# Performance work log

Hardware: AMD Instinct MI355X
Metric: run time of the kernel (lower is better)

The kernel has to match this reference:

```python
import jax, jax.numpy as jnp
import numpy as np

KS = 3        # kernel_size
STRIDE = 1    # patch_stride
RATE = 2      # compression_rate
SCALE = 10.0  # softmax_scale
FUSE_K = 3    # fuse_kernel
EPS = 1e-9
RAW_K = 2 * RATE


def _pad_same(x, k, stride, dilation):
    # TF-style SAME zero padding, matching the torch module's same_pad.
    H, W = x.shape[-2], x.shape[-1]
    oh, ow = -(-H // stride), -(-W // stride)
    eff = (k - 1) * dilation + 1
    ph = max(0, (oh - 1) * stride + eff - H)
    pw = max(0, (ow - 1) * stride + eff - W)
    pads = [(0, 0)] * (x.ndim - 2) + [(ph // 2, ph - ph // 2), (pw // 2, pw - pw // 2)]
    return jnp.pad(x, pads), oh, ow


def extract_patches(x, k, stride, dilation):
    # x: [B,C,H,W] -> [B, L, C, k, k]; L row-major over output grid (== torch Unfold + view/permute)
    xp, oh, ow = _pad_same(x, k, stride, dilation)
    B, C = x.shape[0], x.shape[1]
    cols = [xp[:, :,
               i * dilation: i * dilation + (oh - 1) * stride + 1: stride,
               j * dilation: j * dilation + (ow - 1) * stride + 1: stride]
            for i in range(k) for j in range(k)]
    p = jnp.stack(cols, axis=2).reshape(B, C, k, k, oh * ow)
    return p.transpose(0, 4, 1, 2, 3), oh, ow


def _diag_fuse(x):
    # SAME conv of a 2D map with an eye(FUSE_K) kernel == sum of FUSE_K diagonal shifts.
    pad = FUSE_K - 1
    t = pad // 2
    xp = jnp.pad(x, ((t, pad - t), (t, pad - t)))
    return sum(xp[d:d + x.shape[0], d:d + x.shape[1]] for d in range(FUSE_K))


def _forward(fg, bg, mask):
    B, C, H, W = fg.shape
    # raw (full-res) background patches -> transpose-conv reconstruction weights  [B,L,C,4,4]
    wr, _, _ = extract_patches(bg, RAW_K, RATE * STRIDE, RATE)
    # nearest downsample by RATE (torch F.interpolate nearest, scale 1/RATE)
    fgd = fg[:, :, ::RATE, ::RATE]
    bgd = bg[:, :, ::RATE, ::RATE]
    hd, wd = fgd.shape[2], fgd.shape[3]
    # matching weights from downsampled background  [B,L,C,3,3]
    w, _, _ = extract_patches(bgd, KS, STRIDE, 1)
    # mask resized (nearest) to downsampled grid, patch means  [B,L]
    md = mask[:, :, ::H // hd, ::W // wd]
    mp, _, _ = extract_patches(md, KS, STRIDE, 1)
    m = jnp.mean(mp, axis=(2, 3, 4))
    # foreground patches (SAME, stride 1) for the dynamic-weight conv  [B,Lf,C,3,3]
    fp, _, _ = extract_patches(fgd, KS, 1, 1)

    def per_sample(fp_i, w_i, wr_i, m_i):
        # L2-normalize each background patch (eps added per element, as in torch code)
        norm = jnp.sqrt(jnp.sum(w_i ** 2 + EPS, axis=(1, 2, 3), keepdims=True))
        wn = w_i / norm
        # conv2d(fg, weight) == patch-matching GEMM: sim[l, q] over fg positions q
        sim = jnp.einsum('qcij,lcij->lq', fp_i, wn)  # [L, Lf]
        # fuse: diagonal smoothing along both (bg-patch, fg-pixel) axis pairings
        s = _diag_fuse(sim)
        s = s.reshape(hd, wd, hd, wd).transpose(1, 0, 3, 2).reshape(wd * hd, wd * hd)
        s = _diag_fuse(s)
        sim = s.reshape(wd, hd, wd, hd).transpose(1, 0, 3, 2).reshape(hd * wd, hd, wd)
        mi = m_i[:, None, None]
        sim = jax.nn.softmax(sim * mi * SCALE, axis=0) * mi  # softmax over L
        # conv_transpose2d(sim, wr, stride=RATE) via lhs-dilated conv with flipped kernel
        wk = jnp.flip(wr_i, axis=(2, 3)).transpose(1, 0, 2, 3)  # [C, L, 4, 4]
        y = jax.lax.conv_general_dilated(
            sim[None], wk, window_strides=(1, 1),
            padding=[(RAW_K - 1, RAW_K - 1)] * 2,
            lhs_dilation=(RATE, RATE),
            dimension_numbers=('NCHW', 'OIHW', 'NCHW'))
        return y[0, :, :H, :W] / float(RAW_K ** 2)

    return jax.vmap(per_sample)(fp, w, wr, m)  # [B, C, H, W]


def setup_inputs() -> dict:
    key = jax.random.key(0)
    k1, k2, k3 = jax.random.split(key, 3)
    B, C, H, W = 4, 96, 96, 96
    fg = jax.random.normal(k1, (B, C, H, W), dtype=jnp.float32)
    bg = jax.random.normal(k2, (B, C, H, W), dtype=jnp.float32)
    mask = jnp.round(jax.random.uniform(k3, (B, 1, H, W), dtype=jnp.float32))
    return {"fg": fg, "bg": bg, "mask": mask}


def reference(fg, bg, mask):
    return _forward(fg, bg, mask)
```

## Files before the change

kernel.cpp:

```cpp
#include <hip/hip_runtime.h>
#include <hip/hip_bf16.h>
#include <cstdint>
#include <cstring>

#define ND 48
#define LQ 2304
#define CCH 96
#define HWD 96
#define CHW (CCH*HWD*HWD)
#define HW2 (HWD*HWD)
#define K2P 2560
#define NJ2 384
#define KSP 384

typedef __attribute__((ext_vector_type(8))) short bf16x8;
typedef __attribute__((ext_vector_type(4))) float f32x4;

__device__ __forceinline__ float4 ld4u(const float* p) {
  float4 v; __builtin_memcpy(&v, p, 16); return v;
}

__global__ void k_down(const float* __restrict__ fg, const float* __restrict__ bg,
                       float* __restrict__ fgdT, float* __restrict__ bgdT,
                       float* __restrict__ n2, size_t sd, size_t sp) {
  int b = blockIdx.z;
  const float* fgb = fg + (size_t)b * CHW;
  const float* bgb = bg + (size_t)b * CHW;
  float* fT = fgdT + (size_t)b * sd;
  float* bT = bgdT + (size_t)b * sd;
  float* n2b = n2 + (size_t)b * sp;
  int p = blockIdx.x * 256 + threadIdx.x;
  if (p >= LQ) return;
  int py = p / ND, px = p % ND;
  const float* fsrc = fgb + (2 * py) * HWD + 2 * px;
  const float* gsrc = bgb + (2 * py) * HWD + 2 * px;
  float s = 0.f;
  for (int c = 0; c < CCH; ++c) {
    float f = fsrc[c * HW2];
    float g = gsrc[c * HW2];
    fT[c * LQ + p] = f;
    bT[c * LQ + p] = g;
    s += g * g;
  }
  n2b[p] = s;
}

__global__ void k_aux(const float* __restrict__ n2, const float* __restrict__ mask,
                      float* __restrict__ rnorm, float* __restrict__ mval, size_t sp) {
  int b = blockIdx.z;
  const float* n2b = n2 + (size_t)b * sp;
  const float* mb = mask + (size_t)b * HW2;
  float* rn = rnorm + (size_t)b * sp;
  float* mv = mval + (size_t)b * sp;
  int p = blockIdx.x * 256 + threadIdx.x;
  if (p >= LQ) return;
  int py = p / ND, px = p % ND;
  float ssq = 0.f, ms = 0.f;
  for (int dy = -1; dy <= 1; ++dy)
    for (int dx = -1; dx <= 1; ++dx) {
      int yy = py + dy, xx = px + dx;
      if (yy >= 0 && yy < ND && xx >= 0 && xx < ND) {
        ssq += n2b[yy * ND + xx];
        ms  += mb[(2 * yy) * HWD + 2 * xx];
      }
    }
  rn[p] = 1.0f / sqrtf(ssq + 864.0f * 1e-9f);
  mv[p] = ms * (1.0f / 9.0f);
}

__global__ __launch_bounds__(256) void k_split(const float* __restrict__ fgdT,
                                               const float* __restrict__ bgdT,
                                               __hip_bfloat16* __restrict__ AB,
                                               size_t sd, size_t sAB) {
  int b = blockIdx.z;
  const float* fT = fgdT + (size_t)b * sd;
  const float* gT = bgdT + (size_t)b * sd;
  __hip_bfloat16* Ao = AB + (size_t)b * sAB;
  __hip_bfloat16* Bo = Ao + (size_t)LQ * KSP;
  __shared__ float fs[96 * 65], gs[96 * 65];
  int q0 = blockIdx.x * 64;
  int tid = threadIdx.x;
#pragma unroll
  for (int i = 0; i < 24; ++i) {
    int e = i * 256 + tid;
    int c = e >> 6, qq = e & 63;
    fs[c * 65 + qq] = fT[c * LQ + q0 + qq];
    gs[c * 65 + qq] = gT[c * LQ + q0 + qq];
  }
  __syncthreads();
  for (int i = 0; i < 24; ++i) {
    int e = i * 256 + tid;
    int qq = e / 96, k4 = (e % 96) * 4;
    unsigned short a4[4], b4[4];
    if (k4 < 288) {
      int part = k4 / 96, c = k4 % 96;
#pragma unroll
      for (int j = 0; j < 4; ++j) {
        float f = fs[(c + j) * 65 + qq];
        float g = gs[(c + j) * 65 + qq];
        __hip_bfloat16 fh = __float2bfloat16(f);
        __hip_bfloat16 gh = __float2bfloat16(g);
        __hip_bfloat16 fl = __float2bfloat16(f - __bfloat162float(fh));
        __hip_bfloat16 gl = __float2bfloat16(g - __bfloat162float(gh));
        __hip_bfloat16 av = (part == 2) ? fl : fh;
        __hip_bfloat16 bv = (part == 1) ? gl : gh;
        a4[j] = *(unsigned short*)&av;
        b4[j] = *(unsigned short*)&bv;
      }
    } else {
      a4[0] = a4[1] = a4[2] = a4[3] = 0;
      b4[0] = b4[1] = b4[2] = b4[3] = 0;
    }
    __builtin_memcpy(&Ao[(size_t)(q0 + qq) * KSP + k4], a4, 8);
    __builtin_memcpy(&Bo[(size_t)(q0 + qq) * KSP + k4], b4, 8);
  }
}

__device__ __forceinline__ void gload16(const void* g, void* l) {
  __builtin_amdgcn_global_load_lds((const __attribute__((address_space(1))) void*)g,
                                   (__attribute__((address_space(3))) void*)l, 16, 0, 0);
}

__global__ __launch_bounds__(256) void k_rgemm_mfma(const __hip_bfloat16* __restrict__ AB,
                                                    float* __restrict__ R,
                                                    size_t sAB, size_t sR) {
  int bz = blockIdx.z;
  const __hip_bfloat16* Aq = AB + (size_t)bz * sAB;
  const __hip_bfloat16* Bq = Aq + (size_t)LQ * KSP;
  float* Rb = R + (size_t)bz * sR;
  __shared__ __align__(16) __hip_bfloat16 As[2][64 * 128];
  __shared__ __align__(16) __hip_bfloat16 Bs[2][64 * 128];
  int m0 = blockIdx.y * 64, n0 = blockIdx.x * 64;
  int tid = threadIdx.x;
  int w = tid >> 6, lane = tid & 63;
  int wm = w >> 1, wn = w & 1;
  f32x4 acc[2][2] = {};

  auto STAGE = [&](int buf, int k0) {
#pragma unroll
    for (int i = 0; i < 4; ++i) {
      int g = i * 256 + tid;
      int row = g >> 4, slot = g & 15;
      int ks = 8 * (slot ^ (row & 7));
      gload16(Aq + (size_t)(m0 + row) * KSP + k0 + ks, &As[buf][g * 8]);
      gload16(Bq + (size_t)(n0 + row) * KSP + k0 + ks, &Bs[buf][g * 8]);
    }
  };

  STAGE(0, 0);
  __syncthreads();
  int cur = 0;
  for (int t = 0; t < 3; ++t) {
    if (t + 1 < 3) STAGE(cur ^ 1, (t + 1) * 128);
#pragma unroll
    for (int kk = 0; kk < 128; kk += 32) {
      bf16x8 af[2], bfr[2];
#pragma unroll
      for (int mi = 0; mi < 2; ++mi) {
        int row = wm * 32 + mi * 16 + (lane & 15);
        int e = (kk + (lane >> 4) * 8) ^ ((row & 7) * 8);
        af[mi] = *(const bf16x8*)(&As[cur][row * 128 + e]);
      }
#pragma unroll
      for (int ni = 0; ni < 2; ++ni) {
        int row = wn * 32 + ni * 16 + (lane & 15);
        int e = (kk + (lane >> 4) * 8) ^ ((row & 7) * 8);
        bfr[ni] = *(const bf16x8*)(&Bs[cur][row * 128 + e]);
      }
#pragma unroll
      for (int mi = 0; mi < 2; ++mi)
#pragma unroll
        for (int ni = 0; ni < 2; ++ni)
          acc[mi][ni] = __builtin_amdgcn_mfma_f32_16x16x32_bf16(af[mi], bfr[ni], acc[mi][ni], 0, 0, 0);
    }
    __syncthreads();
    cur ^= 1;
  }

#pragma unroll
  for (int mi = 0; mi < 2; ++mi)
#pragma unroll
    for (int ni = 0; ni < 2; ++ni)
#pragma unroll
      for (int rr = 0; rr < 4; ++rr) {
        int row = m0 + wm * 32 + mi * 16 + (lane >> 4) * 4 + rr;
        int col = n0 + wn * 32 + ni * 16 + (lane & 15);
        Rb[(size_t)row * LQ + col] = acc[mi][ni][rr];
      }
}

__global__ void k_t9v(const float* __restrict__ R, const float* __restrict__ rnorm,
                      float* __restrict__ A2, size_t sR, size_t sp) {
  int b = blockIdx.z;
  const float* S = R + (size_t)b * sR;
  const float* rn = rnorm + (size_t)b * sp;
  float* O = A2 + (size_t)b * sR;
  int bid = blockIdx.x;
  int wg = (bid & 7) * 648 + (bid >> 3);
  int t = wg * 256 + threadIdx.x;
  int id = t * 4;
  int q = id / LQ, l = id % LQ;
  int qy = q / ND, qx = q % ND;
  int ly = l / ND, lx0 = l % ND;
  float4 acc = make_float4(0.f, 0.f, 0.f, 0.f);
#pragma unroll
  for (int dy = -1; dy <= 1; ++dy) {
    if (qy + dy < 0 || qy + dy >= ND || ly + dy < 0 || ly + dy >= ND) continue;
#pragma unroll
    for (int dx = -1; dx <= 1; ++dx) {
      if (qx + dx < 0 || qx + dx >= ND) continue;
      int off = (dy * ND + dx) * (LQ + 1);
      float4 m = ld4u(S + id + off);
      if (dx == -1 && lx0 == 0) m.x = 0.f;
      if (dx == 1 && lx0 == ND - 4) m.w = 0.f;
      acc.x += m.x; acc.y += m.y; acc.z += m.z; acc.w += m.w;
    }
  }
  float4 r4 = *(const float4*)(rn + l);
  acc.x *= r4.x; acc.y *= r4.y; acc.z *= r4.z; acc.w *= r4.w;
  *(float4*)(O + id) = acc;
}

__global__ void k_fusev(const float* __restrict__ A2, float* __restrict__ F, size_t sR) {
  int b = blockIdx.z;
  const float* S = A2 + (size_t)b * sR;
  float* Fo = F + (size_t)b * sR;
  int bid = blockIdx.x;
  int wg = (bid & 7) * 648 + (bid >> 3);
  int t = wg * 256 + threadIdx.x;
  int id = t * 4;
  int a = id / LQ, bc0 = id % LQ;
  float4 c = *(const float4*)(S + id);
  if (a > 0) {
    float4 m = ld4u(S + id - LQ - 1);
    if (bc0 == 0) m.x = 0.f;
    c.x += m.x; c.y += m.y; c.z += m.z; c.w += m.w;
  }
  if (a < LQ - 1) {
    float4 p = ld4u(S + id + LQ + 1);
    if (bc0 == LQ - 4) p.w = 0.f;
    c.x += p.x; c.y += p.y; c.z += p.z; c.w += p.w;
  }
  *(float4*)(Fo + id) = c;
}

__global__ __launch_bounds__(256) void k_softmax(const float* __restrict__ F,
                                                 const float* __restrict__ mval,
                                                 __hip_bfloat16* __restrict__ P50s,
                                                 size_t sR, size_t sp, size_t sP) {
  int b = blockIdx.z;
  const float* Fb = F + (size_t)b * sR;
  const float* mv = mval + (size_t)b * sp;
  __hip_bfloat16* Pb = P50s + (size_t)b * sP + K2P;
  int bid = blockIdx.x;
  int q = (bid & 7) * 288 + (bid >> 3);
  int qy = q / ND, qx = q % ND;
  int tid = threadIdx.x;
  __shared__ float wred[8];
  int fq0 = qx * ND + qy - 1, fq2 = qx * ND + qy + 1;
  bool qok0 = (fq0 >= 0), qok2 = (fq2 < LQ);
  const float* pm = Fb + (size_t)(qok0 ? (fq0 % ND) * ND + fq0 / ND : 0) * LQ;
  const float* pc = Fb + (size_t)q * LQ;
  const float* pp = Fb + (size_t)(qok2 ? (fq2 % ND) * ND + fq2 / ND : 0) * LQ;

  float lg[3][4], mq[3][4];
  float vmax = -1e30f;
#pragma unroll
  for (int s = 0; s < 3; ++s) {
    int Qi = s * 256 + tid;
    bool act = (Qi < 576);
    if (act) {
      int l = Qi * 4;
      int ly = l / ND, lx0 = l % ND;
      float4 acc = *(const float4*)(pc + l);
      if (qok0) {
        float4 t0 = (ly > 0) ? ld4u(pm + l - ND) : ld4u(pm + 2255 + lx0);
        if (ly == 0 && lx0 == 0) t0.x = 0.f;
        acc.x += t0.x; acc.y += t0.y; acc.z += t0.z; acc.w += t0.w;
      }
      if (qok2) {
        float4 t2 = (ly < ND - 1) ? ld4u(pp + l + ND) : ld4u(pp + lx0 + 1);
        if (ly == ND - 1 && lx0 == ND - 4) t2.w = 0.f;
        acc.x += t2.x; acc.y += t2.y; acc.z += t2.z; acc.w += t2.w;
      }
      float4 m4 = *(const float4*)(mv + l);
      mq[s][0] = m4.x; mq[s][1] = m4.y; mq[s][2] = m4.z; mq[s][3] = m4.w;
      lg[s][0] = acc.x * 10.0f * m4.x;
      lg[s][1] = acc.y * 10.0f * m4.y;
      lg[s][2] = acc.z * 10.0f * m4.z;
      lg[s][3] = acc.w * 10.0f * m4.w;
#pragma unroll
      for (int j = 0; j < 4; ++j) vmax = fmaxf(vmax, lg[s][j]);
    } else {
#pragma unroll
      for (int j = 0; j < 4; ++j) { lg[s][j] = -1e30f; mq[s][j] = 0.f; }
    }
  }
#pragma unroll
  for (int d = 32; d; d >>= 1) vmax = fmaxf(vmax, __shfl_xor(vmax, d));
  int wv = tid >> 6, lane = tid & 63;
  if (lane == 0) wred[wv] = vmax;
  __syncthreads();
  vmax = fmaxf(fmaxf(wred[0], wred[1]), fmaxf(wred[2], wred[3]));
  float ssum = 0.f;
#pragma unroll
  for (int s = 0; s < 3; ++s)
#pragma unroll
    for (int j = 0; j < 4; ++j) { lg[s][j] = __expf(lg[s][j] - vmax); ssum += lg[s][j]; }
#pragma unroll
  for (int d = 32; d; d >>= 1) ssum += __shfl_xor(ssum, d);
  if (lane == 0) wred[4 + wv] = ssum;
  __syncthreads();
  float inv = 1.0f / (wred[4] + wred[5] + wred[6] + wred[7]);
#pragma unroll
  for (int s = 0; s < 3; ++s) {
    int Qi = s * 256 + tid;
    if (Qi >= 576) continue;
    int l = Qi * 4;
    int ly = l / ND;
    size_t base = (size_t)q * K2P + l + 2 * ly;
    unsigned int u01, u23;
    {
      __hip_bfloat16 h0 = __float2bfloat16(lg[s][0] * inv * mq[s][0]);
      __hip_bfloat16 h1 = __float2bfloat16(lg[s][1] * inv * mq[s][1]);
      unsigned short s0, s1;
      __builtin_memcpy(&s0, &h0, 2); __builtin_memcpy(&s1, &h1, 2);
      u01 = (unsigned int)s0 | ((unsigned int)s1 << 16);
      __hip_bfloat16 h2 = __float2bfloat16(lg[s][2] * inv * mq[s][2]);
      __hip_bfloat16 h3 = __float2bfloat16(lg[s][3] * inv * mq[s][3]);
      unsigned short s2, s3;
      __builtin_memcpy(&s2, &h2, 2); __builtin_memcpy(&s3, &h3, 2);
      u23 = (unsigned int)s2 | ((unsigned int)s3 << 16);
    }
    *(unsigned int*)((unsigned short*)Pb + base) = u01;
    *(unsigned int*)((unsigned short*)Pb + base + 2) = u23;
  }
  __hip_bfloat16 z = __float2bfloat16(0.f);
  int pc2;
  if (tid < 96)        pc2 = (tid >> 1) * 50 + ND + (tid & 1);
  else if (tid < 196)  pc2 = 2400 + (tid - 96);
  else                 pc2 = 2500 + (tid - 196);
  Pb[(size_t)q * K2P + pc2] = z;
  if (q == 0)
    for (int i = tid; i < K2P; i += 256) (Pb - K2P)[i] = z;
}

__global__ void k_q2v(const __hip_bfloat16* __restrict__ P50s,
                      __hip_bfloat16* __restrict__ Q2, size_t sP, size_t sQ) {
  int bz = blockIdx.z;
  const __hip_bfloat16* P = P50s + (size_t)bz * sP + K2P;
  __hip_bfloat16* Q = Q2 + (size_t)bz * sQ;
  int bid = blockIdx.x;
  int wg = (bid & 7) * 360 + (bid >> 3);
  int id = wg * 256 + threadIdx.x;
  int r = id / 320, c8 = (id % 320) * 8;
  int a = r / ND, b = r % ND;
  const __hip_bfloat16* base = P + (size_t)r * K2P + c8;
  float acc[8];
  {
    unsigned short s[8]; __builtin_memcpy(s, base, 16);
#pragma unroll
    for (int i = 0; i < 8; ++i) {
      unsigned int u = ((unsigned int)s[i]) << 16;
      acc[i] = __builtin_bit_cast(float, u);
    }
  }
  if (b >= 1) {
    unsigned short s[8]; __builtin_memcpy(s, base - (K2P + 2), 16);
#pragma unroll
    for (int i = 0; i < 8; ++i) {
      unsigned int u = ((unsigned int)s[i]) << 16;
      acc[i] += __builtin_bit_cast(float, u);
    }
  }
  if (a >= 1) {
    unsigned short s[8]; __builtin_memcpy(s, base - (ND * K2P + 100), 16);
#pragma unroll
    for (int i = 0; i < 8; ++i) {
      unsigned int u = ((unsigned int)s[i]) << 16;
      acc[i] += __builtin_bit_cast(float, u);
    }
  }
  if (a >= 1 && b >= 1) {
    unsigned short s[8]; __builtin_memcpy(s, base - ((ND + 1) * K2P + 102), 16);
#pragma unroll
    for (int i = 0; i < 8; ++i) {
      unsigned int u = ((unsigned int)s[i]) << 16;
      acc[i] += __builtin_bit_cast(float, u);
    }
  }
  __hip_bfloat16 o[8];
#pragma unroll
  for (int i = 0; i < 8; ++i) o[i] = __float2bfloat16(acc[i]);
  *(bf16x8*)(Q + (size_t)r * K2P + c8) = *(bf16x8*)o;
}

__global__ void k_b2(const float* __restrict__ bgdT, __hip_bfloat16* __restrict__ B2,
                     size_t sd, size_t sB) {
  int b = blockIdx.z;
  const float* gT = bgdT + (size_t)b * sd;
  __hip_bfloat16* Bb = B2 + (size_t)b * sB;
  int id = blockIdx.x * 256 + threadIdx.x;
  if (id >= NJ2 * K2P) return;
  int j = id / K2P, col = id % K2P;
  int c = j >> 2, s = (j >> 1) & 1, t = j & 1;
  float v = 0.f;
  if (col < 2500) {
    int m = col / 50, n = col % 50;
    int ry = m + s - 1, rx = n + t - 1;
    if (ry >= 0 && ry < ND && rx >= 0 && rx < ND)
      v = gT[c * LQ + ry * ND + rx];
  }
  Bb[id] = __float2bfloat16(v);
}

__global__ __launch_bounds__(256) void k_gemm3(const __hip_bfloat16* __restrict__ A,
                                               const __hip_bfloat16* __restrict__ B,
                                               float* __restrict__ out,
                                               size_t sQ, size_t sB) {
  int bz = blockIdx.z;
  const __hip_bfloat16* Ab = A + (size_t)bz * sQ;
  const __hip_bfloat16* Bb = B + (size_t)bz * sB;
  float* ob = out + (size_t)bz * CHW;
  int wg = (blockIdx.x & 7) * 27 + (blockIdx.x >> 3);
  int n0 = (wg % 6) * 64, m0 = (wg / 6) * 64;
  __shared__ __align__(16) __hip_bfloat16 As[2][64 * 64];
  __shared__ __align__(16) __hip_bfloat16 Bs[2][64 * 64];
  int tid = threadIdx.x;
  int w = tid >> 6, lane = tid & 63;
  int wm = w >> 1, wn = w & 1;
  int l3 = lane >> 3, l7 = lane & 7;
  int kswz = (l7 * 8) ^ (l3 << 3);
  f32x4 acc[2][2] = {};

  auto STAGE = [&](int buf, int k0) {
#pragma unroll
    for (int i = 0; i < 2; ++i) {
      int chunk = w * 2 + i;
      int row = chunk * 8 + l3;
      gload16(Ab + (size_t)(m0 + row) * K2P + k0 + kswz, &As[buf][chunk * 8 * 64]);
      gload16(Bb + (size_t)(n0 + row) * K2P + k0 + kswz, &Bs[buf][chunk * 8 * 64]);
    }
  };

  STAGE(0, 0);
  __syncthreads();
  int cur = 0;
  constexpr int NT = K2P / 64;
  for (int t = 0; t < NT; ++t) {
    if (t + 1 < NT) STAGE(cur ^ 1, (t + 1) * 64);
#pragma unroll
    for (int kk = 0; kk < 64; kk += 32) {
      bf16x8 af[2], bfr[2];
#pragma unroll
      for (int mi = 0; mi < 2; ++mi) {
        int row = wm * 32 + mi * 16 + (lane & 15);
        int e = (kk + (lane >> 4) * 8) ^ ((row & 7) * 8);
        af[mi] = *(const bf16x8*)(&As[cur][row * 64 + e]);
      }
#pragma unroll
      for (int ni = 0; ni < 2; ++ni) {
        int row = wn * 32 + ni * 16 + (lane & 15);
        int e = (kk + (lane >> 4) * 8) ^ ((row & 7) * 8);
        bfr[ni] = *(const bf16x8*)(&Bs[cur][row * 64 + e]);
      }
#pragma unroll
      for (int mi = 0; mi < 2; ++mi)
#pragma unroll
        for (int ni = 0; ni < 2; ++ni)
          acc[mi][ni] = __builtin_amdgcn_mfma_f32_16x16x32_bf16(af[mi], bfr[ni], acc[mi][ni], 0, 0, 0);
    }
    __syncthreads();
    cur ^= 1;
  }

#pragma unroll
  for (int mi = 0; mi < 2; ++mi)
#pragma unroll
    for (int ni = 0; ni < 2; ++ni)
#pragma unroll
      for (int rr = 0; rr < 4; ++rr) {
        int r_ = m0 + wm * 32 + mi * 16 + (lane >> 4) * 4 + rr;
        int j  = n0 + wn * 32 + ni * 16 + (lane & 15);
        int a = r_ / ND, bcol = r_ % ND;
        int c = j >> 2, s = (j >> 1) & 1, tt = j & 1;
        ob[((size_t)c * HWD + 2 * a + s) * HWD + 2 * bcol + tt] = acc[mi][ni][rr] * 0.0625f;
      }
}

extern "C" void kernel_launch(void* const* d_in, const int* in_sizes, int n_in,
                              void* d_out, int out_size, void* d_ws, size_t ws_size,
                              hipStream_t stream) {
  const float* fg_all = (const float*)d_in[0];
  const float* bg_all = (const float*)d_in[1];
  const float* mask_all = (const float*)d_in[2];
  float* out_all = (float*)d_out;
  float* ws = (float*)d_ws;

  int B = in_sizes[0] / CHW;

  const size_t S_D = (size_t)CCH * LQ;
  const size_t S_P = LQ;
  const size_t S_R = (size_t)LQ * LQ;
  const size_t S_P50 = (size_t)(LQ + 1) * K2P;
  const size_t per_floats = S_D * 2 + S_P * 3 + S_R * 2 + S_P50 / 2;

  bool batched = ws_size >= (size_t)B * per_floats * 4;
  int na = batched ? B : 1;
  int nb = na;

  float* fgdT  = ws;
  float* bgdT  = fgdT + (size_t)na * S_D;
  float* n2    = bgdT + (size_t)na * S_D;
  float* rnorm = n2 + (size_t)na * S_P;
  float* mval  = rnorm + (size_t)na * S_P;
  float* bufA  = mval + (size_t)na * S_P;
  float* bufB  = bufA + (size_t)na * S_R;
  __hip_bfloat16* P50 = (__hip_bfloat16*)(bufB + (size_t)na * S_R);
  __hip_bfloat16* Q2  = (__hip_bfloat16*)bufA;
  __hip_bfloat16* B2  = (__hip_bfloat16*)bufB;
  __hip_bfloat16* ABs = P50;

  size_t sd = batched ? S_D : 0, sp = batched ? S_P : 0, sR = batched ? S_R : 0;
  size_t sP = batched ? S_P50 : 0;
  size_t sQ = batched ? S_R * 2 : 0;
  size_t sB = batched ? S_R * 2 : 0;

  for (int b0 = 0; b0 < B; b0 += nb) {
    const float* fg = fg_all + (size_t)(batched ? 0 : b0) * CHW;
    const float* bg = bg_all + (size_t)(batched ? 0 : b0) * CHW;
    const float* mask = mask_all + (size_t)(batched ? 0 : b0) * HW2;
    float* out = out_all + (size_t)(batched ? 0 : b0) * CHW;

    hipLaunchKernelGGL(k_down, dim3(9, 1, nb), dim3(256), 0, stream,
                       fg, bg, fgdT, bgdT, n2, sd, sp);
    hipLaunchKernelGGL(k_aux, dim3(9, 1, nb), dim3(256), 0, stream,
                       n2, mask, rnorm, mval, sp);
    hipLaunchKernelGGL(k_split, dim3(36, 1, nb), dim3(256), 0, stream,
                       fgdT, bgdT, ABs, sd, sP);
    hipLaunchKernelGGL(k_rgemm_mfma, dim3(36, 36, nb), dim3(256), 0, stream,
                       ABs, bufA, sP, sR);
    hipLaunchKernelGGL(k_t9v, dim3(5184, 1, nb), dim3(256), 0, stream,
                       bufA, rnorm, bufB, sR, sp);
    hipLaunchKernelGGL(k_fusev, dim3(5184, 1, nb), dim3(256), 0, stream,
                       bufB, bufA, sR);
    hipLaunchKernelGGL(k_softmax, dim3(2304, 1, nb), dim3(256), 0, stream,
                       bufA, mval, P50, sR, sp, sP);
    hipLaunchKernelGGL(k_q2v, dim3(2880, 1, nb), dim3(256), 0, stream,
                       P50, Q2, sP, sQ);
    hipLaunchKernelGGL(k_b2, dim3(3840, 1, nb), dim3(256), 0, stream,
                       bgdT, B2, sd, sB);
    hipLaunchKernelGGL(k_gemm3, dim3(216, 1, nb), dim3(256), 0, stream,
                       Q2, B2, out, sQ, sB);
  }
}
```

Baseline: 243.9 us.

## Fuse 3x3 patch-sum and diagonal fuse into a single stencil kernel

Merges the 3x3 similarity window sum (with rnorm scaling) and the diagonal fuse pass into one kernel. Each thread loads a 3x5 neighbourhood of float4 values once and forms all three diagonal-shifted window sums from registers, with a scalar slow path near row edges. This removes one full 2304x2304-per-batch intermediate write and read plus a launch, at the cost of more loads per thread, more registers and complex boundary logic.

```diff
diff --git a/kernel.cpp b/kernel.cpp
--- a/kernel.cpp
+++ b/kernel.cpp
@@ -189,59 +189,94 @@
       }
 }
 
-__global__ void k_t9v(const float* __restrict__ R, const float* __restrict__ rnorm,
-                      float* __restrict__ A2, size_t sR, size_t sp) {
-  int b = blockIdx.z;
-  const float* S = R + (size_t)b * sR;
-  const float* rn = rnorm + (size_t)b * sp;
-  float* O = A2 + (size_t)b * sR;
+__global__ void k_tf(const float* __restrict__ R, const float* __restrict__ rnorm,
+                     float* __restrict__ F, size_t sR, size_t sp) {
+  int bz = blockIdx.z;
+  const float* S = R + (size_t)bz * sR;
+  const float* rn = rnorm + (size_t)bz * sp;
+  float* Fo = F + (size_t)bz * sR;
   int bid = blockIdx.x;
   int wg = (bid & 7) * 648 + (bid >> 3);
   int t = wg * 256 + threadIdx.x;
   int id = t * 4;
-  int q = id / LQ, l = id % LQ;
-  int qy = q / ND, qx = q % ND;
-  int ly = l / ND, lx0 = l % ND;
+  int a = id / LQ, b = id % LQ;
+  int ay = a / ND, ax = a % ND;
+  int by = b / ND, bx0 = b % ND;
+
+  float4 L[3][5];
+#pragma unroll
+  for (int r = 0; r < 3; ++r)
+#pragma unroll
+    for (int c = 0; c < 5; ++c)
+      L[r][c] = ld4u(S + id + ((r - 1) * ND + (c - 2)) * (LQ + 1));
+
   float4 acc = make_float4(0.f, 0.f, 0.f, 0.f);
-#pragma unroll
-  for (int dy = -1; dy <= 1; ++dy) {
-    if (qy + dy < 0 || qy + dy >= ND || ly + dy < 0 || ly + dy >= ND) continue;
-#pragma unroll
-    for (int dx = -1; dx <= 1; ++dx) {
-      if (qx + dx < 0 || qx + dx >= ND) continue;
-      int off = (dy * ND + dx) * (LQ + 1);
-      float4 m = ld4u(S + id + off);
-      if (dx == -1 && lx0 == 0) m.x = 0.f;
-      if (dx == 1 && lx0 == ND - 4) m.w = 0.f;
-      acc.x += m.x; acc.y += m.y; acc.z += m.z; acc.w += m.w;
-    }
-  }
-  float4 r4 = *(const float4*)(rn + l);
-  acc.x *= r4.x; acc.y *= r4.y; acc.z *= r4.z; acc.w *= r4.w;
-  *(float4*)(O + id) = acc;
-}
-
-__global__ void k_fusev(const float* __restrict__ A2, float* __restrict__ F, size_t sR) {
-  int b = blockIdx.z;
-  const float* S = A2 + (size_t)b * sR;
-  float* Fo = F + (size_t)b * sR;
-  int bid = blockIdx.x;
-  int wg = (bid & 7) * 648 + (bid >> 3);
-  int t = wg * 256 + threadIdx.x;
-  int id = t * 4;
-  int a = id / LQ, bc0 = id % LQ;
-  float4 c = *(const float4*)(S + id);
-  if (a > 0) {
-    float4 m = ld4u(S + id - LQ - 1);
-    if (bc0 == 0) m.x = 0.f;
-    c.x += m.x; c.y += m.y; c.z += m.z; c.w += m.w;
-  }
-  if (a < LQ - 1) {
-    float4 p = ld4u(S + id + LQ + 1);
-    if (bc0 == LQ - 4) p.w = 0.f;
-    c.x += p.x; c.y += p.y; c.z += p.z; c.w += p.w;
-  }
-  *(float4*)(Fo + id) = c;
+
+  if (bx0 >= 4 && bx0 <= ND - 8) {
+#pragma unroll
+    for (int dd = 0; dd < 3; ++dd) {
+      int d = dd - 1;
+      bool flat = (d < 0) ? (a > 0) : ((d > 0) ? (a < LQ - 1) : true);
+      int py = ay, px = ax + d;
+      if (px < 0) { px = ND - 1; py = ay - 1; }
+      else if (px >= ND) { px = 0; py = ay + 1; }
+      float4 t9 = make_float4(0.f, 0.f, 0.f, 0.f);
+#pragma unroll
+      for (int yy = 0; yy < 3; ++yy) {
+        int dy = yy - 1;
+        bool oky = flat && (py + dy >= 0) && (py + dy < ND)
+                        && (by + dy >= 0) && (by + dy < ND);
+#pragma unroll
+        for (int xx = 0; xx < 3; ++xx) {
+          int dx = xx - 1;
+          bool ok = oky && (px + dx >= 0) && (px + dx < ND);
+          if (ok) {
+            float4 Lv = L[yy][dx + d + 2];
+            t9.x += Lv.x; t9.y += Lv.y; t9.z += Lv.z; t9.w += Lv.w;
+          }
+        }
+      }
+      float4 r4 = ld4u(rn + b + d);
+      acc.x += r4.x * t9.x; acc.y += r4.y * t9.y;
+      acc.z += r4.z * t9.z; acc.w += r4.w * t9.w;
+    }
+  } else {
+    float av[4] = {0.f, 0.f, 0.f, 0.f};
+#pragma unroll
+    for (int dd = 0; dd < 3; ++dd) {
+      int d = dd - 1;
+      int p = a + d;
+      if (p < 0 || p >= LQ) continue;
+      int py = ay, px = ax + d;
+      if (px < 0) { px = ND - 1; py = ay - 1; }
+      else if (px >= ND) { px = 0; py = ay + 1; }
+#pragma unroll
+      for (int j = 0; j < 4; ++j) {
+        int m = b + j + d;
+        if (m < 0 || m >= LQ) continue;
+        int tt = bx0 + j + d;
+        int my = by, mx = tt;
+        if (tt < 0) { my = by - 1; mx = tt + ND; }
+        else if (tt >= ND) { my = by + 1; mx = tt - ND; }
+        float s9 = 0.f;
+#pragma unroll
+        for (int yy = 0; yy < 3; ++yy) {
+          int dy = yy - 1;
+          if (py + dy < 0 || py + dy >= ND || my + dy < 0 || my + dy >= ND) continue;
+#pragma unroll
+          for (int xx = 0; xx < 3; ++xx) {
+            int dx = xx - 1;
+            if (px + dx < 0 || px + dx >= ND || mx + dx < 0 || mx + dx >= ND) continue;
+            const float* lv = (const float*)&L[yy][dx + d + 2];
+            s9 += lv[j];
+          }
+        }
+        av[j] += rn[m] * s9;
+      }
+    }
+    acc = make_float4(av[0], av[1], av[2], av[3]);
+  }
+  *(float4*)(Fo + id) = acc;
 }
 
 __global__ __launch_bounds__(256) void k_softmax(const float* __restrict__ F,
@@ -540,12 +575,10 @@
                        fgdT, bgdT, ABs, sd, sP);
     hipLaunchKernelGGL(k_rgemm_mfma, dim3(36, 36, nb), dim3(256), 0, stream,
                        ABs, bufA, sP, sR);
-    hipLaunchKernelGGL(k_t9v, dim3(5184, 1, nb), dim3(256), 0, stream,
+    hipLaunchKernelGGL(k_tf, dim3(5184, 1, nb), dim3(256), 0, stream,
                        bufA, rnorm, bufB, sR, sp);
-    hipLaunchKernelGGL(k_fusev, dim3(5184, 1, nb), dim3(256), 0, stream,
-                       bufB, bufA, sR);
     hipLaunchKernelGGL(k_softmax, dim3(2304, 1, nb), dim3(256), 0, stream,
-                       bufA, mval, P50, sR, sp, sP);
+                       bufB, mval, P50, sR, sp, sP);
     hipLaunchKernelGGL(k_q2v, dim3(2880, 1, nb), dim3(256), 0, stream,
                        P50, Q2, sP, sQ);
     hipLaunchKernelGGL(k_b2, dim3(3840, 1, nb), dim3(256), 0, stream,
```

Result: slower. 301.5 us (+23.6%).
